# Kernel optimization log

Measured on AMD Instinct MI355X. Metric: run time of the kernel, lower is better.

Reference implementation:

```python
import jax, jax.numpy as jnp
import numpy as np

B, S, D, H, FF = 4, 2048, 1024, 16, 4096
HD = D // H


def setup_inputs() -> dict:
    key = jax.random.key(0)
    ks = jax.random.split(key, 12)
    s = 1.0 / np.sqrt(D)
    sf = 1.0 / np.sqrt(FF)
    return {
        "x": jax.random.normal(ks[0], (B, S, D), dtype=jnp.float32),
        "lengths": jax.random.randint(ks[1], (B,), 1, S + 1, dtype=jnp.int32),
        "qW": jax.random.uniform(ks[2], (D, D), jnp.float32, -s, s),
        "qb": jnp.zeros((D,), jnp.float32),
        "kW": jax.random.uniform(ks[3], (D, D), jnp.float32, -s, s),
        "kb": jnp.zeros((D,), jnp.float32),
        "vW": jax.random.uniform(ks[4], (D, D), jnp.float32, -s, s),
        "vb": jnp.zeros((D,), jnp.float32),
        "oW": jax.random.uniform(ks[5], (D, D), jnp.float32, -s, s),
        "ob": jnp.zeros((D,), jnp.float32),
        "w1": jax.random.uniform(ks[6], (D, FF), jnp.float32, -s, s),
        "b1": jnp.zeros((FF,), jnp.float32),
        "w2": jax.random.uniform(ks[7], (FF, D), jnp.float32, -sf, sf),
        "b2": jnp.zeros((D,), jnp.float32),
    }


def _heads(t):
    # [B,S,D] -> [B,H,S,HD]
    return t.reshape(B, S, H, HD).transpose(0, 2, 1, 3)


def reference(x, lengths, qW, qb, kW, kb, vW, vb, oW, ob, w1, b1, w2, b2):
    q = _heads(x @ qW + qb)
    k = _heads(x @ kW + kb)
    v = _heads(x @ vW + vb)
    scale = 1.0 / np.sqrt(HD)
    logits = jnp.einsum("bhqd,bhkd->bhqk", q, k) * scale  # [B,H,S,S]
    # key-position mask: pos >= length -> -inf
    mask = jnp.arange(S)[None, None, None, :] >= lengths[:, None, None, None]
    logits = jnp.where(mask, -jnp.inf, logits)
    a = jax.nn.softmax(logits, axis=-1)
    ctx = jnp.einsum("bhqk,bhkd->bhqd", a, v)
    ctx = ctx.transpose(0, 2, 1, 3).reshape(B, S, D)
    attn_out = ctx @ oW + ob
    h = jax.nn.relu(attn_out @ w1 + b1)
    return h @ w2 + b2
```

## Files before the change

### kernel.cpp

```cpp
#include <hip/hip_runtime.h>


typedef short bf16x8 __attribute__((ext_vector_type(8)));
typedef float f32x4 __attribute__((ext_vector_type(4)));

__device__ __forceinline__ unsigned short f2bf(float f) {
  unsigned int u = __builtin_bit_cast(unsigned int, f);
  u += 0x7fffu + ((u >> 16) & 1u);
  return (unsigned short)(u >> 16);
}

__device__ __forceinline__ void gload16(const unsigned short* g, unsigned short* l) {
  __builtin_amdgcn_global_load_lds(
      (const __attribute__((address_space(1))) unsigned int*)(g),
      (__attribute__((address_space(3))) unsigned int*)(l),
      16, 0, 0);
}

__global__ __launch_bounds__(256) void cast_f32_bf16(
    const float* __restrict__ src, unsigned short* __restrict__ dst, int n4) {
  int i = blockIdx.x * 256 + threadIdx.x;
  if (i < n4) {
    float4 f = ((const float4*)src)[i];
    ushort4 o;
    o.x = f2bf(f.x); o.y = f2bf(f.y); o.z = f2bf(f.z); o.w = f2bf(f.w);
    ((ushort4*)dst)[i] = o;
  }
}

__global__ __launch_bounds__(256) void prep_weights(
    const float* __restrict__ qW, const float* __restrict__ kW,
    const float* __restrict__ vW, const float* __restrict__ oW,
    const float* __restrict__ w1, const float* __restrict__ w2,
    unsigned short* __restrict__ qWt, unsigned short* __restrict__ kWt,
    unsigned short* __restrict__ vWt, unsigned short* __restrict__ oWt,
    unsigned short* __restrict__ w1t, unsigned short* __restrict__ w2t) {
  const int t = blockIdx.x;
  const float* W; unsigned short* Wt; int N, K, nt, kt;
  if (t < 2048) {
    const int w = t >> 9, r = t & 511;
    nt = r & 15; kt = r >> 4; N = 1024; K = 1024;
    W  = w == 0 ? qW : w == 1 ? kW : w == 2 ? vW : oW;
    Wt = w == 0 ? qWt : w == 1 ? kWt : w == 2 ? vWt : oWt;
  } else if (t < 4096) {
    const int r = t - 2048;
    nt = r & 63; kt = r >> 6; N = 4096; K = 1024; W = w1; Wt = w1t;
  } else {
    const int r = t - 4096;
    nt = r & 15; kt = r >> 4; N = 1024; K = 4096; W = w2; Wt = w2t;
  }
  const int wave = threadIdx.x >> 6, lane = threadIdx.x & 63;
  const int n = nt * 64 + lane;
  const int k0 = kt * 32 + wave * 8;
  union { int4 v; unsigned short u[8]; } s;
#pragma unroll
  for (int j = 0; j < 8; ++j) s.u[j] = f2bf(W[(size_t)(k0 + j) * N + n]);
  *(int4*)(Wt + (size_t)n * K + k0) = s.v;
}

__device__ __forceinline__ void gemm256_8ph(
    const unsigned short* __restrict__ A, const unsigned short* __restrict__ Bt,
    unsigned short* __restrict__ As, unsigned short* __restrict__ Bs,
    const int m0, const int n0, const int K, f32x4 (&acc)[8][4]) {
  const int tid = (int)threadIdx.x;
  const int w = tid >> 6, l = tid & 63;
  const int quad = l >> 4, l16 = l & 15;
  const int wm = (w >> 2) * 128, wn = (w & 3) * 64;

  const int srow = w * 8 + (l >> 3);
  const int schunk = ((l & 7) ^ (l >> 3)) * 8;
  const unsigned short* gA = A + (size_t)(m0 + srow) * K + schunk;
  const unsigned short* gB = Bt + (size_t)(n0 + srow) * K + schunk;
  const int ldsW = w * 512;

  const int xr = l16 & 7;
  const int c0 = ((0 + quad) ^ xr) * 8;
  const int c1 = ((4 + quad) ^ xr) * 8;

  bf16x8 af[4][2], bf0[2][2], bf1[2][2];

  auto STA = [&](int buf, int a, int t) {
    gload16(gA + (size_t)(a * 64) * K + t * 64,
            As + buf * 16384 + a * 4096 + ldsW);
  };
  auto STB = [&](int buf, int a, int t) {
    gload16(gB + (size_t)(a * 64) * K + t * 64,
            Bs + buf * 16384 + a * 4096 + ldsW);
  };
  auto LDA = [&](int buf, int mh) {
    const unsigned short* p = As + buf * 16384 + (wm + mh * 64 + l16) * 64;
#pragma unroll
    for (int mi = 0; mi < 4; ++mi) {
      af[mi][0] = *(const bf16x8*)(p + mi * 16 * 64 + c0);
      af[mi][1] = *(const bf16x8*)(p + mi * 16 * 64 + c1);
    }
  };
  auto LDB = [&](int buf, int nh, bf16x8 (&bf)[2][2]) {
    const unsigned short* p = Bs + buf * 16384 + (wn + nh * 32 + l16) * 64;
#pragma unroll
    for (int ni = 0; ni < 2; ++ni) {
      bf[ni][0] = *(const bf16x8*)(p + ni * 16 * 64 + c0);
      bf[ni][1] = *(const bf16x8*)(p + ni * 16 * 64 + c1);
    }
  };
  auto MM = [&](int mh, int nh, bf16x8 (&bf)[2][2]) {
    __builtin_amdgcn_s_setprio(1);
#pragma unroll
    for (int mi = 0; mi < 4; ++mi)
#pragma unroll
      for (int ni = 0; ni < 2; ++ni) {
        f32x4& a = acc[mh * 4 + mi][nh * 2 + ni];
        a = __builtin_amdgcn_mfma_f32_16x16x32_bf16(af[mi][0], bf[ni][0], a, 0, 0, 0);
        a = __builtin_amdgcn_mfma_f32_16x16x32_bf16(af[mi][1], bf[ni][1], a, 0, 0, 0);
      }
    __builtin_amdgcn_s_setprio(0);
  };

  const int NK = K >> 6;
  STB(0, 0, 0); STB(0, 1, 0); STB(0, 2, 0); STB(0, 3, 0);
  STA(0, 0, 0); STA(0, 2, 0); STA(0, 1, 0); STA(0, 3, 0);
  asm volatile("s_waitcnt vmcnt(2)" ::: "memory");
  __builtin_amdgcn_s_barrier();

#pragma unroll 1
  for (int t = 0; t < NK; ++t) {
    const int c = t & 1, nb = c ^ 1;
    const bool st = (t + 1 < NK);
    LDA(c, 0); LDB(c, 0, bf0);
    if (st) { STB(nb, 0, t + 1); STB(nb, 1, t + 1); }
    __builtin_amdgcn_s_barrier();
    asm volatile("s_waitcnt lgkmcnt(0)" ::: "memory");
    __builtin_amdgcn_sched_barrier(0);
    MM(0, 0, bf0);
    __builtin_amdgcn_s_barrier();
    LDB(c, 1, bf1);
    if (st) { STB(nb, 2, t + 1); STB(nb, 3, t + 1); }
    __builtin_amdgcn_s_barrier();
    asm volatile("s_waitcnt lgkmcnt(0)" ::: "memory");
    __builtin_amdgcn_sched_barrier(0);
    MM(0, 1, bf1);
    if (st) asm volatile("s_waitcnt vmcnt(4)" ::: "memory");
    else    asm volatile("s_waitcnt vmcnt(0)" ::: "memory");
    __builtin_amdgcn_s_barrier();
    LDA(c, 1);
    if (st) { STA(nb, 0, t + 1); STA(nb, 2, t + 1); }
    __builtin_amdgcn_s_barrier();
    asm volatile("s_waitcnt lgkmcnt(0)" ::: "memory");
    __builtin_amdgcn_sched_barrier(0);
    MM(1, 1, bf1);
    __builtin_amdgcn_s_barrier();
    if (st) { STA(nb, 1, t + 1); STA(nb, 3, t + 1); }
    __builtin_amdgcn_s_barrier();
    MM(1, 0, bf0);
    if (st) asm volatile("s_waitcnt vmcnt(2)" ::: "memory");
    __builtin_amdgcn_s_barrier();
  }
}

template <int EPI>
__global__ __launch_bounds__(512, 1) void gemm256_bt(
    const unsigned short* __restrict__ A, const unsigned short* __restrict__ Bt,
    const float* __restrict__ bias, void* __restrict__ C, int N, int K) {
  __shared__ unsigned short As[2 * 16384];
  __shared__ unsigned short Bs[2 * 16384];
  const int tn = N >> 8;
  const int cpx = (int)gridDim.x >> 3;
  const int sw = ((int)blockIdx.x & 7) * cpx + ((int)blockIdx.x >> 3);
  const int nt = sw % tn, mt = sw / tn;
  const int m0 = mt * 256, n0 = nt * 256;

  f32x4 acc[8][4] = {};
  gemm256_8ph(A, Bt, As, Bs, m0, n0, K, acc);

  const int tid = (int)threadIdx.x;
  const int w = tid >> 6, l = tid & 63;
  const int quad = l >> 4, l16 = l & 15;
  const int wm = (w >> 2) * 128, wn = (w & 3) * 64;

  if (EPI == 0) {
#pragma unroll
    for (int ni = 0; ni < 4; ++ni) {
      const int col = n0 + wn + ni * 16 + l16;
      const float bv = bias[col];
#pragma unroll
      for (int mi = 0; mi < 8; ++mi) {
        const int row = m0 + wm + mi * 16 + quad * 4;
#pragma unroll
        for (int r = 0; r < 4; ++r)
          ((float*)C)[(size_t)(row + r) * N + col] = acc[mi][ni][r] + bv;
      }
    }
    return;
  }

  __syncthreads();
  unsigned short* sc = (w < 4) ? (As + w * 4608) : (Bs + (w - 4) * 4608);
  const int rr8 = l >> 3, c8 = (l & 7) * 8;
#pragma unroll
  for (int half = 0; half < 2; ++half) {
#pragma unroll
    for (int ni = 0; ni < 4; ++ni) {
      const int col = n0 + wn + ni * 16 + l16;
      const float bv = bias[col];
#pragma unroll
      for (int mi2 = 0; mi2 < 4; ++mi2) {
#pragma unroll
        for (int r = 0; r < 4; ++r) {
          float v = acc[half * 4 + mi2][ni][r] + bv;
          if (EPI == 2) v = v > 0.f ? v : 0.f;
          sc[(mi2 * 16 + quad * 4 + r) * 72 + ni * 16 + l16] = f2bf(v);
        }
      }
    }
    __syncthreads();
#pragma unroll
    for (int i = 0; i < 8; ++i) {
      bf16x8 vv = *(const bf16x8*)(sc + (i * 8 + rr8) * 72 + c8);
      const int row = m0 + wm + half * 64 + i * 8 + rr8;
      *(bf16x8*)((unsigned short*)C + (size_t)row * N + n0 + wn + c8) = vv;
    }
    __syncthreads();
  }
}

__device__ __forceinline__ void gemm128_core(
    const unsigned short* __restrict__ A, const unsigned short* __restrict__ Bt,
    unsigned short* __restrict__ As, unsigned short* __restrict__ Bs,
    const int m0, const int n0, const int K, f32x4 (&acc)[4][4]) {
  const int tid = (int)threadIdx.x;
  const int w = tid >> 6, l = tid & 63;
  const int quad = l >> 4, l16 = l & 15;
  const int wm = (w >> 1) * 64, wn = (w & 1) * 64;

  const int lr = l >> 2, lc = l & 3;
  const int swz = (lc ^ ((l >> 3) & 3)) * 8;
  const unsigned short* gA[2]; const unsigned short* gB[2];
  unsigned short* dA[2]; unsigned short* dB[2];
#pragma unroll
  for (int j = 0; j < 2; ++j) {
    const int rr = (w * 2 + j) * 16 + lr;
    gA[j] = A + (size_t)(m0 + rr) * K + swz;
    gB[j] = Bt + (size_t)(n0 + rr) * K + swz;
    dA[j] = As + (w * 2 + j) * 512;
    dB[j] = Bs + (w * 2 + j) * 512;
  }

  const int cread = (quad ^ ((l16 >> 1) & 3)) * 8;
  const int rA = (wm + l16) * 32;
  const int rB = (wn + l16) * 32;

  auto STAGE = [&](int db, int t) {
#pragma unroll
    for (int j = 0; j < 2; ++j) {
      gload16(gA[j] + t * 32, dA[j] + db * 4096);
      gload16(gB[j] + t * 32, dB[j] + db * 4096);
    }
  };
  auto DSR = [&](int db, bf16x8 (&af)[4], bf16x8 (&bf)[4]) {
    const unsigned short* pa = As + db * 4096 + rA + cread;
    const unsigned short* pb = Bs + db * 4096 + rB + cread;
#pragma unroll
    for (int ni = 0; ni < 4; ++ni) bf[ni] = *(const bf16x8*)(pb + ni * 16 * 32);
#pragma unroll
    for (int mi = 0; mi < 4; ++mi) af[mi] = *(const bf16x8*)(pa + mi * 16 * 32);
  };
  auto MM = [&](bf16x8 (&af)[4], bf16x8 (&bf)[4]) {
    __builtin_amdgcn_s_setprio(1);
#pragma unroll
    for (int mi = 0; mi < 4; ++mi)
#pragma unroll
      for (int ni = 0; ni < 4; ++ni)
        acc[mi][ni] = __builtin_amdgcn_mfma_f32_16x16x32_bf16(
            af[mi], bf[ni], acc[mi][ni], 0, 0, 0);
    __builtin_amdgcn_s_setprio(0);
  };

  bf16x8 afA[4], bfA[4], afB[4], bfB[4];

  const int NK = K >> 5;
  STAGE(0, 0); STAGE(1, 1); STAGE(2, 2);
  asm volatile("s_waitcnt vmcnt(8)" ::: "memory");
  __builtin_amdgcn_s_barrier();
  DSR(0, afA, bfA);

#define STEP128(T, afC, bfC, afN, bfN)                                \
  {                                                                   \
    const int t_ = (T);                                               \
    if (t_ + 2 < NK) asm volatile("s_waitcnt vmcnt(4)" ::: "memory"); \
    else             asm volatile("s_waitcnt vmcnt(0)" ::: "memory"); \
    __builtin_amdgcn_s_barrier();                                     \
    DSR((t_ + 1) & 3, afN, bfN);                                      \
    if (t_ + 3 < NK) STAGE((t_ + 3) & 3, t_ + 3);                     \
    MM(afC, bfC);                                                     \
  }

#pragma unroll 1
  for (int t = 0; t < NK - 2; t += 2) {
    STEP128(t, afA, bfA, afB, bfB);
    STEP128(t + 1, afB, bfB, afA, bfA);
  }
  STEP128(NK - 2, afA, bfA, afB, bfB);
  MM(afB, bfB);
#undef STEP128
}

template <int EPI>
__global__ __launch_bounds__(256, 2) void gemm128_bt(
    const unsigned short* __restrict__ A, const unsigned short* __restrict__ Bt,
    const float* __restrict__ bias, void* __restrict__ C, int N, int K) {
  __shared__ unsigned short As[4 * 4096];
  __shared__ unsigned short Bs[4 * 4096];
  const int NT = N >> 7, band = NT >> 3;
  const int xcd = blockIdx.x & 7, local = blockIdx.x >> 3;
  const int nt = xcd * band + local % band;
  const int mt = local / band;
  const int m0 = mt * 128, n0 = nt * 128;

  f32x4 acc[4][4] = {};
  gemm128_core(A, Bt, As, Bs, m0, n0, K, acc);

  const int tid = (int)threadIdx.x;
  const int w = tid >> 6, l = tid & 63;
  const int quad = l >> 4, l16 = l & 15;
  const int wm = (w >> 1) * 64, wn = (w & 1) * 64;

  if (EPI == 0) {
#pragma unroll
    for (int ni = 0; ni < 4; ++ni) {
      const int col = n0 + wn + ni * 16 + l16;
      const float bv = bias[col];
#pragma unroll
      for (int mi = 0; mi < 4; ++mi) {
        const int row = m0 + wm + mi * 16 + quad * 4;
#pragma unroll
        for (int r = 0; r < 4; ++r)
          ((float*)C)[(size_t)(row + r) * N + col] = acc[mi][ni][r] + bv;
      }
    }
    return;
  }

  __syncthreads();
  unsigned short* sc = (w < 2) ? (As + w * 4608) : (Bs + (w - 2) * 4608);
  const int rr8 = l >> 3, c8 = (l & 7) * 8;
#pragma unroll
  for (int ni = 0; ni < 4; ++ni) {
    const int col = n0 + wn + ni * 16 + l16;
    const float bv = bias[col];
#pragma unroll
    for (int mi = 0; mi < 4; ++mi) {
#pragma unroll
      for (int r = 0; r < 4; ++r) {
        float v = acc[mi][ni][r] + bv;
        if (EPI == 2) v = v > 0.f ? v : 0.f;
        sc[(mi * 16 + quad * 4 + r) * 72 + ni * 16 + l16] = f2bf(v);
      }
    }
  }
  __syncthreads();
#pragma unroll
  for (int i = 0; i < 8; ++i) {
    bf16x8 vv = *(const bf16x8*)(sc + (i * 8 + rr8) * 72 + c8);
    const int row = m0 + wm + i * 8 + rr8;
    *(bf16x8*)((unsigned short*)C + (size_t)row * N + n0 + wn + c8) = vv;
  }
}

#define QSCALE 0.180336884f

__global__ __launch_bounds__(256, 2) void gemm128_qkv(
    const unsigned short* __restrict__ A, const unsigned short* __restrict__ Bt,
    const float* __restrict__ qb, const float* __restrict__ kb,
    const float* __restrict__ vb, unsigned short* __restrict__ Qo,
    unsigned short* __restrict__ Ko, unsigned short* __restrict__ Vto, int K) {
  __shared__ unsigned short As[4 * 4096];
  __shared__ unsigned short Bs[4 * 4096];
  const int NT = 24, band = 3;
  const int xcd = blockIdx.x & 7, local = blockIdx.x >> 3;
  const int nt = xcd * band + local % band;
  const int mt = local / band;
  const int m0 = mt * 128, n0 = nt * 128;

  f32x4 acc[4][4] = {};
  gemm128_core(A, Bt, As, Bs, m0, n0, K, acc);

  const int tid = (int)threadIdx.x;
  const int w = tid >> 6, l = tid & 63;
  const int quad = l >> 4, l16 = l & 15;
  const int wm = (w >> 1) * 64, wn = (w & 1) * 64;

  const int seg = n0 >> 10;
  const float* bias = seg == 0 ? qb : (seg == 1 ? kb : vb);
  const int colb = (n0 + wn) & 1023;

  __syncthreads();
  unsigned short* sc = (w < 2) ? (As + w * 4608) : (Bs + (w - 2) * 4608);
  const int rr8 = l >> 3, c8 = (l & 7) * 8;

  if (seg == 2) {
    const int b = m0 >> 11;
    const int hh = colb >> 6;
    const int s0 = (m0 & 2047) + wm;
#pragma unroll
    for (int ni = 0; ni < 4; ++ni) {
      const float bv = bias[colb + ni * 16 + l16];
#pragma unroll
      for (int mi = 0; mi < 4; ++mi) {
        union { ushort4 v; unsigned short u[4]; } pk;
#pragma unroll
        for (int r = 0; r < 4; ++r) pk.u[r] = f2bf(acc[mi][ni][r] + bv);
        *(ushort4*)(sc + (ni * 16 + l16) * 72 + mi * 16 + quad * 4) = pk.v;
      }
    }
    __syncthreads();
    unsigned short* vbase = Vto + ((size_t)(b * 16 + hh) * 64) * 2048;
#pragma unroll
    for (int i = 0; i < 8; ++i) {
      bf16x8 vv = *(const bf16x8*)(sc + (i * 8 + rr8) * 72 + c8);
      const int dh = i * 8 + rr8;
      *(bf16x8*)(vbase + (size_t)dh * 2048 + s0 + c8) = vv;
    }
  } else {
    unsigned short* Out = seg == 0 ? Qo : Ko;
#pragma unroll
    for (int ni = 0; ni < 4; ++ni) {
      const float bv = bias[colb + ni * 16 + l16];
#pragma unroll
      for (int mi = 0; mi < 4; ++mi) {
#pragma unroll
        for (int r = 0; r < 4; ++r) {
          float v = acc[mi][ni][r] + bv;
          if (seg == 0) v *= QSCALE;
          sc[(mi * 16 + quad * 4 + r) * 72 + ni * 16 + l16] = f2bf(v);
        }
      }
    }
    __syncthreads();
#pragma unroll
    for (int i = 0; i < 8; ++i) {
      bf16x8 vv = *(const bf16x8*)(sc + (i * 8 + rr8) * 72 + c8);
      const int row = m0 + wm + i * 8 + rr8;
      *(bf16x8*)(Out + (size_t)row * 1024 + colb + c8) = vv;
    }
  }
}

__global__ __launch_bounds__(256, 4) void attn_fused(
    const unsigned short* __restrict__ Q, const unsigned short* __restrict__ K,
    const unsigned short* __restrict__ Vt, const int* __restrict__ lengths,
    unsigned short* __restrict__ ctx) {
  constexpr int S = 2048, D = 1024;
  __shared__ unsigned short Ks[64 * 72];
  __shared__ unsigned short Vs[64 * 72];
  __shared__ unsigned short Ps[4 * 32 * 72];

  const int tid = threadIdx.x;
  const int wave = tid >> 6, lane = tid & 63;
  const int quad = lane >> 4, l16 = lane & 15;
  const int bid = blockIdx.x;
  const int qt = bid & 15;
  const int h = (bid >> 4) & 15;
  const int b = bid >> 8;
  const int q0 = qt * 128;
  const int len = lengths[b];
  const int ktEnd = (len + 63) >> 6;
  const float NEGINF = -__builtin_inff();

  const size_t xbase = (size_t)b * S * D + (size_t)h * 64;
  const size_t vtb = (size_t)(b * 16 + h) * 64;

  bf16x8 qf0[2], qf1[2];
#pragma unroll
  for (int mb = 0; mb < 2; ++mb) {
    const unsigned short* qrow =
        Q + xbase + (size_t)(q0 + wave * 32 + mb * 16 + l16) * D;
    qf0[mb] = *(const bf16x8*)(qrow + quad * 8);
    qf1[mb] = *(const bf16x8*)(qrow + 32 + quad * 8);
  }

  const int sr1 = tid >> 3, sc1 = (tid & 7) * 8;
  const int sr2 = (256 + tid) >> 3, sc2 = (tid & 7) * 8;
  const unsigned short* kg1 = K + xbase + (size_t)sr1 * D + sc1;
  const unsigned short* kg2 = K + xbase + (size_t)sr2 * D + sc2;
  const unsigned short* vg1 = Vt + (vtb + sr1) * S + sc1;
  const unsigned short* vg2 = Vt + (vtb + sr2) * S + sc2;

  f32x4 oacc[2][4] = {};
  float rs[2][4] = {};

  unsigned short* pw = Ps + wave * (32 * 72);

  int4 kr1, kr2, vr1, vr2;
  {
    kr1 = *(const int4*)(kg1);
    kr2 = *(const int4*)(kg2);
    vr1 = *(const int4*)(vg1);
    vr2 = *(const int4*)(vg2);
  }

  for (int kt = 0; kt < ktEnd; ++kt) {
    const int k0 = kt * 64;
    __syncthreads();
    *(int4*)(Ks + sr1 * 72 + sc1) = kr1;
    *(int4*)(Ks + sr2 * 72 + sc2) = kr2;
    *(int4*)(Vs + sr1 * 72 + sc1) = vr1;
    *(int4*)(Vs + sr2 * 72 + sc2) = vr2;
    __syncthreads();

    if (kt + 1 < ktEnd) {
      const int kn = (kt + 1) * 64;
      kr1 = *(const int4*)(kg1 + (size_t)kn * D);
      kr2 = *(const int4*)(kg2 + (size_t)kn * D);
      vr1 = *(const int4*)(vg1 + kn);
      vr2 = *(const int4*)(vg2 + kn);
    }

    f32x4 sf[2][4];
#pragma unroll
    for (int cb = 0; cb < 4; ++cb) {
      const bf16x8 kf0 = *(const bf16x8*)(Ks + (cb * 16 + l16) * 72 + quad * 8);
      const bf16x8 kf1 = *(const bf16x8*)(Ks + (cb * 16 + l16) * 72 + 32 + quad * 8);
#pragma unroll
      for (int mb = 0; mb < 2; ++mb) {
        f32x4 c = {0.f, 0.f, 0.f, 0.f};
        c = __builtin_amdgcn_mfma_f32_16x16x32_bf16(qf0[mb], kf0, c, 0, 0, 0);
        c = __builtin_amdgcn_mfma_f32_16x16x32_bf16(qf1[mb], kf1, c, 0, 0, 0);
        sf[mb][cb] = c;
      }
    }

    if (k0 + 64 > len) {
#pragma unroll
      for (int cb = 0; cb < 4; ++cb) {
        const bool msk = (k0 + cb * 16 + l16) >= len;
#pragma unroll
        for (int mb = 0; mb < 2; ++mb)
#pragma unroll
          for (int r = 0; r < 4; ++r) sf[mb][cb][r] = msk ? NEGINF : sf[mb][cb][r];
      }
    }

#pragma unroll
    for (int mb = 0; mb < 2; ++mb)
#pragma unroll
      for (int cb = 0; cb < 4; ++cb)
#pragma unroll
        for (int r = 0; r < 4; ++r) {
          const float p = __builtin_amdgcn_exp2f(sf[mb][cb][r]);
          sf[mb][cb][r] = p;
          rs[mb][r] += p;
        }

#pragma unroll
    for (int mb = 0; mb < 2; ++mb)
#pragma unroll
      for (int cb = 0; cb < 4; ++cb)
#pragma unroll
        for (int r = 0; r < 4; ++r)
          pw[(mb * 16 + quad * 4 + r) * 72 + cb * 16 + l16] = f2bf(sf[mb][cb][r]);

    bf16x8 pa0[2], pa1[2];
#pragma unroll
    for (int mb = 0; mb < 2; ++mb) {
      pa0[mb] = *(const bf16x8*)(pw + (mb * 16 + l16) * 72 + quad * 8);
      pa1[mb] = *(const bf16x8*)(pw + (mb * 16 + l16) * 72 + 32 + quad * 8);
    }
#pragma unroll
    for (int cb = 0; cb < 4; ++cb) {
      const bf16x8 vb0 = *(const bf16x8*)(Vs + (cb * 16 + l16) * 72 + quad * 8);
      const bf16x8 vb1 = *(const bf16x8*)(Vs + (cb * 16 + l16) * 72 + 32 + quad * 8);
#pragma unroll
      for (int mb = 0; mb < 2; ++mb) {
        oacc[mb][cb] = __builtin_amdgcn_mfma_f32_16x16x32_bf16(pa0[mb], vb0, oacc[mb][cb], 0, 0, 0);
        oacc[mb][cb] = __builtin_amdgcn_mfma_f32_16x16x32_bf16(pa1[mb], vb1, oacc[mb][cb], 0, 0, 0);
      }
    }
  }

#pragma unroll
  for (int off = 8; off > 0; off >>= 1)
#pragma unroll
    for (int mb = 0; mb < 2; ++mb)
#pragma unroll
      for (int r = 0; r < 4; ++r) rs[mb][r] += __shfl_xor(rs[mb][r], off, 16);

#pragma unroll
  for (int mb = 0; mb < 2; ++mb) {
    float inv[4];
#pragma unroll
    for (int r = 0; r < 4; ++r) inv[r] = 1.0f / rs[mb][r];
#pragma unroll
    for (int cb = 0; cb < 4; ++cb)
#pragma unroll
      for (int r = 0; r < 4; ++r) {
        const int row = q0 + wave * 32 + mb * 16 + quad * 4 + r;
        ctx[xbase + (size_t)row * D + cb * 16 + l16] = f2bf(oacc[mb][cb][r] * inv[r]);
      }
  }
}

extern "C" void kernel_launch(void* const* d_in, const int* in_sizes, int n_in,
                              void* d_out, int out_size, void* d_ws,
                              size_t ws_size, hipStream_t stream) {
  const float* x  = (const float*)d_in[0];
  const int* lengths = (const int*)d_in[1];
  const float* qW = (const float*)d_in[2];
  const float* qb = (const float*)d_in[3];
  const float* kW = (const float*)d_in[4];
  const float* kb = (const float*)d_in[5];
  const float* vW = (const float*)d_in[6];
  const float* vb = (const float*)d_in[7];
  const float* oW = (const float*)d_in[8];
  const float* ob = (const float*)d_in[9];
  const float* w1 = (const float*)d_in[10];
  const float* b1 = (const float*)d_in[11];
  const float* w2 = (const float*)d_in[12];
  const float* b2 = (const float*)d_in[13];
  float* out = (float*)d_out;

  const int Bx = 4, S = 2048, D = 1024, FF = 4096;
  const int M = Bx * S;

  unsigned short* p = (unsigned short*)d_ws;
  unsigned short* xb  = p; p += (size_t)M * D;
  unsigned short* qWt = p; p += (size_t)D * D;
  unsigned short* kWt = p; p += (size_t)D * D;
  unsigned short* vWt = p; p += (size_t)D * D;
  unsigned short* oWt = p; p += (size_t)D * D;
  unsigned short* w1t = p; p += (size_t)D * FF;
  unsigned short* w2t = p; p += (size_t)FF * D;
  unsigned short* Qb  = p; p += (size_t)M * D;
  unsigned short* Kb  = p; p += (size_t)M * D;
  unsigned short* Vtb = p; p += (size_t)M * D;
  unsigned short* Cb  = p; p += (size_t)M * D;
  unsigned short* Ab  = p; p += (size_t)M * D;
  unsigned short* Hb  = p; p += (size_t)M * FF;

  {
    int n4 = (int)((size_t)M * D / 4);
    cast_f32_bf16<<<dim3((n4 + 255) / 256), dim3(256), 0, stream>>>(x, xb, n4);
  }
  prep_weights<<<dim3(6144), dim3(256), 0, stream>>>(
      qW, kW, vW, oW, w1, w2, qWt, kWt, vWt, oWt, w1t, w2t);

  gemm128_qkv<<<dim3(1536), dim3(256), 0, stream>>>(
      xb, qWt, qb, kb, vb, Qb, Kb, Vtb, D);

  attn_fused<<<dim3(Bx * 16 * (S / 128)), dim3(256), 0, stream>>>(
      Qb, Kb, Vtb, lengths, Cb);

  gemm128_bt<1><<<dim3(512), dim3(256), 0, stream>>>(Cb, oWt, ob, Ab, D, D);
  gemm256_bt<2><<<dim3(512), dim3(512), 0, stream>>>(Ab, w1t, b1, Hb, FF, D);
  gemm128_bt<0><<<dim3(512), dim3(256), 0, stream>>>(Hb, w2t, b2, out, D, FF);
}
```

Before: 450.2 us.

## Use BK=32 triple-buffered pipeline in 256 GEMM and retile XCD block mapping

The 256x256 GEMM core switches from double-buffered BK=64 stages to triple-buffered BK=32 stages, prefetching two k-steps ahead with a new LDS swizzle and one MFMA per fragment pair. The block-to-tile mappings of the 256 GEMM, the 128 GEMM and the QKV GEMM are rewritten so each XCD owns a 2D rectangle of output tiles, aiming for better L2 reuse. The extra prefetch depth is meant to hide global latency, at the cost of twice as many k-iterations and barriers. The new mappings hardcode grid shapes, so they assume specific N and M sizes.

```diff
diff --git a/kernel.cpp b/kernel.cpp
--- a/kernel.cpp
+++ b/kernel.cpp
@@ -58,7 +58,7 @@
   *(int4*)(Wt + (size_t)n * K + k0) = s.v;
 }
 
-__device__ __forceinline__ void gemm256_8ph(
+__device__ __forceinline__ void gemm256_core(
     const unsigned short* __restrict__ A, const unsigned short* __restrict__ Bt,
     unsigned short* __restrict__ As, unsigned short* __restrict__ Bs,
     const int m0, const int n0, const int K, f32x4 (&acc)[8][4]) {
@@ -67,93 +67,84 @@
   const int quad = l >> 4, l16 = l & 15;
   const int wm = (w >> 2) * 128, wn = (w & 3) * 64;
 
-  const int srow = w * 8 + (l >> 3);
-  const int schunk = ((l & 7) ^ (l >> 3)) * 8;
+  const int srow = w * 16 + (l >> 2);
+  const int schunk = ((l & 3) ^ ((l >> 3) & 3)) * 8;
   const unsigned short* gA = A + (size_t)(m0 + srow) * K + schunk;
   const unsigned short* gB = Bt + (size_t)(n0 + srow) * K + schunk;
-  const int ldsW = w * 512;
-
-  const int xr = l16 & 7;
-  const int c0 = ((0 + quad) ^ xr) * 8;
-  const int c1 = ((4 + quad) ^ xr) * 8;
-
-  bf16x8 af[4][2], bf0[2][2], bf1[2][2];
-
-  auto STA = [&](int buf, int a, int t) {
-    gload16(gA + (size_t)(a * 64) * K + t * 64,
-            As + buf * 16384 + a * 4096 + ldsW);
-  };
-  auto STB = [&](int buf, int a, int t) {
-    gload16(gB + (size_t)(a * 64) * K + t * 64,
-            Bs + buf * 16384 + a * 4096 + ldsW);
-  };
-  auto LDA = [&](int buf, int mh) {
-    const unsigned short* p = As + buf * 16384 + (wm + mh * 64 + l16) * 64;
-#pragma unroll
-    for (int mi = 0; mi < 4; ++mi) {
-      af[mi][0] = *(const bf16x8*)(p + mi * 16 * 64 + c0);
-      af[mi][1] = *(const bf16x8*)(p + mi * 16 * 64 + c1);
-    }
-  };
-  auto LDB = [&](int buf, int nh, bf16x8 (&bf)[2][2]) {
-    const unsigned short* p = Bs + buf * 16384 + (wn + nh * 32 + l16) * 64;
-#pragma unroll
-    for (int ni = 0; ni < 2; ++ni) {
-      bf[ni][0] = *(const bf16x8*)(p + ni * 16 * 64 + c0);
-      bf[ni][1] = *(const bf16x8*)(p + ni * 16 * 64 + c1);
-    }
-  };
-  auto MM = [&](int mh, int nh, bf16x8 (&bf)[2][2]) {
+  const int dsw = w * 512;
+
+  const int cread = (quad ^ ((l16 >> 1) & 3)) * 8;
+
+  auto STA = [&](int buf, int rnd, int t) {
+    gload16(gA + (size_t)(rnd * 128) * K + t * 32,
+            As + buf * 8192 + rnd * 4096 + dsw);
+  };
+  auto STB = [&](int buf, int rnd, int t) {
+    gload16(gB + (size_t)(rnd * 128) * K + t * 32,
+            Bs + buf * 8192 + rnd * 4096 + dsw);
+  };
+  auto LDA4 = [&](int buf, int mh, bf16x8 (&af)[4]) {
+    const unsigned short* p = As + buf * 8192 + (wm + mh * 64 + l16) * 32 + cread;
+#pragma unroll
+    for (int mi = 0; mi < 4; ++mi) af[mi] = *(const bf16x8*)(p + mi * 16 * 32);
+  };
+  auto LDB2 = [&](int buf, int nh, bf16x8 (&bf)[2]) {
+    const unsigned short* p = Bs + buf * 8192 + (wn + nh * 32 + l16) * 32 + cread;
+#pragma unroll
+    for (int ni = 0; ni < 2; ++ni) bf[ni] = *(const bf16x8*)(p + ni * 16 * 32);
+  };
+  auto MM8 = [&](int mh, int nh, bf16x8 (&af)[4], bf16x8 (&bf)[2]) {
     __builtin_amdgcn_s_setprio(1);
 #pragma unroll
     for (int mi = 0; mi < 4; ++mi)
 #pragma unroll
-      for (int ni = 0; ni < 2; ++ni) {
-        f32x4& a = acc[mh * 4 + mi][nh * 2 + ni];
-        a = __builtin_amdgcn_mfma_f32_16x16x32_bf16(af[mi][0], bf[ni][0], a, 0, 0, 0);
-        a = __builtin_amdgcn_mfma_f32_16x16x32_bf16(af[mi][1], bf[ni][1], a, 0, 0, 0);
-      }
+      for (int ni = 0; ni < 2; ++ni)
+        acc[mh * 4 + mi][nh * 2 + ni] = __builtin_amdgcn_mfma_f32_16x16x32_bf16(
+            af[mi], bf[ni], acc[mh * 4 + mi][nh * 2 + ni], 0, 0, 0);
     __builtin_amdgcn_s_setprio(0);
   };
 
-  const int NK = K >> 6;
-  STB(0, 0, 0); STB(0, 1, 0); STB(0, 2, 0); STB(0, 3, 0);
-  STA(0, 0, 0); STA(0, 2, 0); STA(0, 1, 0); STA(0, 3, 0);
-  asm volatile("s_waitcnt vmcnt(2)" ::: "memory");
+  bf16x8 af[4], bf01[2], bf23[2];
+
+  const int NK = K >> 5;
+  STA(0, 0, 0); STA(0, 1, 0); STB(0, 0, 0); STB(0, 1, 0);
+  STA(1, 0, 1); STA(1, 1, 1); STB(1, 0, 1); STB(1, 1, 1);
+  asm volatile("s_waitcnt vmcnt(4)" ::: "memory");
   __builtin_amdgcn_s_barrier();
 
+  int c = 0, cs = 2;
 #pragma unroll 1
   for (int t = 0; t < NK; ++t) {
-    const int c = t & 1, nb = c ^ 1;
-    const bool st = (t + 1 < NK);
-    LDA(c, 0); LDB(c, 0, bf0);
-    if (st) { STB(nb, 0, t + 1); STB(nb, 1, t + 1); }
+    const bool st = (t + 2 < NK);
+    LDA4(c, 0, af); LDB2(c, 0, bf01);
+    if (st) STA(cs, 0, t + 2);
     __builtin_amdgcn_s_barrier();
     asm volatile("s_waitcnt lgkmcnt(0)" ::: "memory");
     __builtin_amdgcn_sched_barrier(0);
-    MM(0, 0, bf0);
-    __builtin_amdgcn_s_barrier();
-    LDB(c, 1, bf1);
-    if (st) { STB(nb, 2, t + 1); STB(nb, 3, t + 1); }
+    MM8(0, 0, af, bf01);
+    __builtin_amdgcn_s_barrier();
+    LDB2(c, 1, bf23);
+    if (st) STA(cs, 1, t + 2);
     __builtin_amdgcn_s_barrier();
     asm volatile("s_waitcnt lgkmcnt(0)" ::: "memory");
     __builtin_amdgcn_sched_barrier(0);
-    MM(0, 1, bf1);
-    if (st) asm volatile("s_waitcnt vmcnt(4)" ::: "memory");
-    else    asm volatile("s_waitcnt vmcnt(0)" ::: "memory");
-    __builtin_amdgcn_s_barrier();
-    LDA(c, 1);
-    if (st) { STA(nb, 0, t + 1); STA(nb, 2, t + 1); }
+    MM8(0, 1, af, bf23);
+    __builtin_amdgcn_s_barrier();
+    LDA4(c, 1, af);
+    if (st) STB(cs, 0, t + 2);
     __builtin_amdgcn_s_barrier();
     asm volatile("s_waitcnt lgkmcnt(0)" ::: "memory");
     __builtin_amdgcn_sched_barrier(0);
-    MM(1, 1, bf1);
-    __builtin_amdgcn_s_barrier();
-    if (st) { STA(nb, 1, t + 1); STA(nb, 3, t + 1); }
-    __builtin_amdgcn_s_barrier();
-    MM(1, 0, bf0);
-    if (st) asm volatile("s_waitcnt vmcnt(2)" ::: "memory");
-    __builtin_amdgcn_s_barrier();
+    MM8(1, 1, af, bf23);
+    __builtin_amdgcn_s_barrier();
+    if (st) STB(cs, 1, t + 2);
+    __builtin_amdgcn_s_barrier();
+    MM8(1, 0, af, bf01);
+    if (st)              asm volatile("s_waitcnt vmcnt(4)" ::: "memory");
+    else if (t + 1 < NK) asm volatile("s_waitcnt vmcnt(0)" ::: "memory");
+    __builtin_amdgcn_s_barrier();
+    c = c == 2 ? 0 : c + 1;
+    cs = cs == 2 ? 0 : cs + 1;
   }
 }
 
@@ -161,16 +152,15 @@
 __global__ __launch_bounds__(512, 1) void gemm256_bt(
     const unsigned short* __restrict__ A, const unsigned short* __restrict__ Bt,
     const float* __restrict__ bias, void* __restrict__ C, int N, int K) {
-  __shared__ unsigned short As[2 * 16384];
-  __shared__ unsigned short Bs[2 * 16384];
-  const int tn = N >> 8;
-  const int cpx = (int)gridDim.x >> 3;
-  const int sw = ((int)blockIdx.x & 7) * cpx + ((int)blockIdx.x >> 3);
-  const int nt = sw % tn, mt = sw / tn;
+  __shared__ unsigned short As[3 * 8192];
+  __shared__ unsigned short Bs[3 * 8192];
+  const int xcd = (int)blockIdx.x & 7, local = (int)blockIdx.x >> 3;
+  const int mt = (xcd >> 1) * 8 + (local >> 3);
+  const int nt = (xcd & 1) * 8 + (local & 7);
   const int m0 = mt * 256, n0 = nt * 256;
 
   f32x4 acc[8][4] = {};
-  gemm256_8ph(A, Bt, As, Bs, m0, n0, K, acc);
+  gemm256_core(A, Bt, As, Bs, m0, n0, K, acc);
 
   const int tid = (int)threadIdx.x;
   const int w = tid >> 6, l = tid & 63;
@@ -310,10 +300,9 @@
     const float* __restrict__ bias, void* __restrict__ C, int N, int K) {
   __shared__ unsigned short As[4 * 4096];
   __shared__ unsigned short Bs[4 * 4096];
-  const int NT = N >> 7, band = NT >> 3;
-  const int xcd = blockIdx.x & 7, local = blockIdx.x >> 3;
-  const int nt = xcd * band + local % band;
-  const int mt = local / band;
+  const int xcd = (int)blockIdx.x & 7, local = (int)blockIdx.x >> 3;
+  const int mt = xcd * 8 + (local >> 3);
+  const int nt = local & 7;
   const int m0 = mt * 128, n0 = nt * 128;
 
   f32x4 acc[4][4] = {};
@@ -375,10 +364,9 @@
     unsigned short* __restrict__ Ko, unsigned short* __restrict__ Vto, int K) {
   __shared__ unsigned short As[4 * 4096];
   __shared__ unsigned short Bs[4 * 4096];
-  const int NT = 24, band = 3;
-  const int xcd = blockIdx.x & 7, local = blockIdx.x >> 3;
-  const int nt = xcd * band + local % band;
-  const int mt = local / band;
+  const int xcd = (int)blockIdx.x & 7, local = (int)blockIdx.x >> 3;
+  const int mt = (xcd >> 1) * 16 + (local & 15);
+  const int nt = (xcd & 1) * 12 + (local >> 4);
   const int m0 = mt * 128, n0 = nt * 128;
 
   f32x4 acc[4][4] = {};
```

Measured after the change: 440.0 us. 1.02x faster.
